# Kernel tuning notes

Measured on AMD Instinct MI355X. Metric: run time of the kernel, lower is better.

## Reference

```python
import jax, jax.numpy as jnp
import numpy as np

H = 2048          # hidden_size
NH = 16           # num attention heads
NKV = 4           # num kv heads (GQA)
HD = 128          # head_dim (= v_head_dim)
E = 16            # n_routed_experts
K = 4             # num_experts_per_tok
DFF = 1024        # moe_intermediate_size
G = 4             # n_group
TG = 2            # topk_group
THETA = 1000000.0
EPS = 1e-6
B, S = 1, 1024


def _rmsnorm(x, w):
    return x * jax.lax.rsqrt(jnp.mean(x * x, axis=-1, keepdims=True) + EPS) * w


def _rope(pos, x):
    # neox-style rotary, full head_dim. x: [B,S,h,HD], pos: [B,S]
    half = HD // 2
    inv_freq = 1.0 / (THETA ** (jnp.arange(half, dtype=jnp.float32) / half))
    ang = pos[..., None].astype(jnp.float32) * inv_freq          # [B,S,half]
    cos = jnp.cos(ang)[:, :, None, :]
    sin = jnp.sin(ang)[:, :, None, :]
    x1, x2 = x[..., :half], x[..., half:]
    return jnp.concatenate([x1 * cos - x2 * sin, x2 * cos + x1 * sin], axis=-1)


def setup_inputs() -> dict:
    key = jax.random.key(0)
    ks = jax.random.split(key, 10)
    sc = 0.02
    return {
        "hidden_states": jax.random.normal(ks[0], (B, S, H), dtype=jnp.float32),
        "positions": jnp.arange(B * S, dtype=jnp.int64 if jax.config.jax_enable_x64 else jnp.int32).reshape(B, S),
        "in_norm_w": jnp.ones((H,), jnp.float32),
        "post_norm_w": jnp.ones((H,), jnp.float32),
        "qkv_w": jax.random.normal(ks[1], (H, (NH + 2 * NKV) * HD), jnp.float32) * sc,
        "o_w": jax.random.normal(ks[2], (NH * HD, H), jnp.float32) * sc,
        "gate_w": jax.random.normal(ks[3], (E, H), jnp.float32) * sc,
        "gate_bias": jax.random.normal(ks[4], (E,), jnp.float32) * sc,
        "gate_up_w": jax.random.normal(ks[5], (E, H, 2 * DFF), jnp.float32) * sc,
        "down_w": jax.random.normal(ks[6], (E, DFF, H), jnp.float32) * sc,
    }


def reference(hidden_states, positions, in_norm_w, post_norm_w, qkv_w, o_w,
              gate_w, gate_bias, gate_up_w, down_w):
    Bq, Sq, _ = hidden_states.shape
    T = Bq * Sq

    # ---- pre-norm attention ----
    residual = hidden_states
    h = _rmsnorm(hidden_states, in_norm_w)
    qkv = h @ qkv_w                                             # [B,S,(NH+2*NKV)*HD]
    q, k, v = jnp.split(qkv, [NH * HD, (NH + NKV) * HD], axis=-1)
    q = q.reshape(Bq, Sq, NH, HD)
    k = k.reshape(Bq, Sq, NKV, HD)
    v = v.reshape(Bq, Sq, NKV, HD)
    q = _rope(positions, q)
    k = _rope(positions, k)
    rep = NH // NKV
    k = jnp.repeat(k, rep, axis=2)                              # [B,S,NH,HD]
    v = jnp.repeat(v, rep, axis=2)
    scores = jnp.einsum('bqhd,bkhd->bhqk', q, k) * (HD ** -0.5)
    causal = jnp.tril(jnp.ones((Sq, Sq), bool))
    scores = jnp.where(causal, scores, -1e30)
    attn = jax.nn.softmax(scores, axis=-1)
    o = jnp.einsum('bhqk,bkhd->bqhd', attn, v).reshape(Bq, Sq, NH * HD)
    h = residual + o @ o_w

    # ---- pre-norm MoE ----
    residual = h
    x = _rmsnorm(h, post_norm_w).reshape(T, H)

    # gate (fp32), sigmoid scores + correction bias, grouped top-k (noaux_tc)
    logits = x.astype(jnp.float32) @ gate_w.T                   # [T,E]
    sig = jax.nn.sigmoid(logits)
    sb = sig + gate_bias.astype(jnp.float32)
    grp = sb.reshape(T, G, E // G)
    group_scores = jax.lax.top_k(grp, 2)[0].sum(-1)             # [T,G]
    _, gidx = jax.lax.top_k(group_scores, TG)
    gmask = jax.nn.one_hot(gidx, G, dtype=sb.dtype).sum(1)      # [T,G]
    emask = jnp.repeat(gmask, E // G, axis=1)                   # [T,E]
    masked = jnp.where(emask > 0, sb, -jnp.inf)
    _, tidx = jax.lax.top_k(masked, K)                          # [T,K]
    w = jnp.take_along_axis(sig, tidx, axis=1)
    w = w / (w.sum(-1, keepdims=True) + 1e-20)                  # renormalize

    # experts: dense compute, sparse combine
    gu = jnp.einsum('td,edf->etf', x, gate_up_w)                # [E,T,2*DFF]
    g, u = jnp.split(gu, 2, axis=-1)
    act = jax.nn.silu(g) * u
    y = jnp.einsum('etf,efd->etd', act, down_w)                 # [E,T,H]
    cw = jnp.zeros((T, E), jnp.float32).at[jnp.arange(T)[:, None], tidx].add(w)
    moe_out = jnp.einsum('te,etd->td', cw, y.astype(jnp.float32))
    return residual + moe_out.astype(hidden_states.dtype).reshape(Bq, Sq, H)
```

## Files before the change

kernel.cpp:

```cpp
#include <hip/hip_runtime.h>
#include <hip/hip_bf16.h>
#include <math.h>

#define H_DIM   2048
#define NH      16
#define NKV     4
#define HD      128
#define NE      16
#define TOPK    4
#define DFF     1024
#define NG      4
#define SEQ     1024
#define QKV_N   3072
#define EPS_RMS 1e-6f
#define THETA   1000000.0f

typedef __attribute__((ext_vector_type(8))) short bf16x8;
typedef __attribute__((ext_vector_type(4))) short s16x4;
typedef __attribute__((ext_vector_type(4))) float f32x4;

__device__ inline unsigned short f2bf(float x) {
    unsigned u = __builtin_bit_cast(unsigned, x);
    unsigned r = (u + 0x7FFFu + ((u >> 16) & 1u)) >> 16;
    return (unsigned short)r;
}

__device__ inline unsigned pk2bf(float lo, float hi) {
    __hip_bfloat162 h = __float22bfloat162_rn(float2{lo, hi});
    unsigned r;
    __builtin_memcpy(&r, &h, 4);
    return r;
}

__global__ __launch_bounds__(256) void w2bfT(const float* __restrict__ in,
                                             unsigned short* __restrict__ out,
                                             int K, int N) {
    const float* src = in + (size_t)blockIdx.z * K * N;
    unsigned short* dst = out + (size_t)blockIdx.z * K * N;
    int n0 = blockIdx.x * 64, k0 = blockIdx.y * 64;
    __shared__ unsigned short tile[64][66];
    int tid = threadIdx.x, c = tid & 63, r4 = tid >> 6;
    #pragma unroll
    for (int rep = 0; rep < 16; rep++) {
        int r = rep * 4 + r4;
        tile[r][c] = f2bf(src[(size_t)(k0 + r) * N + n0 + c]);
    }
    __syncthreads();
    #pragma unroll
    for (int rep = 0; rep < 16; rep++) {
        int r = rep * 4 + r4;
        dst[(size_t)(n0 + r) * K + k0 + c] = tile[c][r];
    }
}

__global__ __launch_bounds__(256) void rmsnorm_dual(const float* __restrict__ in,
                                                    const float* __restrict__ w,
                                                    float* __restrict__ outf,
                                                    unsigned short* __restrict__ outb) {
    int t = blockIdx.x;
    const float* xt = in + (size_t)t * H_DIM;
    float ss = 0.f;
    for (int d = threadIdx.x * 4; d < H_DIM; d += 1024) {
        float4 v = *reinterpret_cast<const float4*>(xt + d);
        ss += v.x * v.x + v.y * v.y + v.z * v.z + v.w * v.w;
    }
    for (int off = 1; off < 64; off <<= 1) ss += __shfl_xor(ss, off);
    __shared__ float red[4];
    __shared__ float srms;
    if ((threadIdx.x & 63) == 0) red[threadIdx.x >> 6] = ss;
    __syncthreads();
    if (threadIdx.x == 0)
        srms = rsqrtf((red[0] + red[1] + red[2] + red[3]) * (1.f / H_DIM) + EPS_RMS);
    __syncthreads();
    float r = srms;
    for (int d = threadIdx.x * 4; d < H_DIM; d += 1024) {
        float4 v  = *reinterpret_cast<const float4*>(xt + d);
        float4 wv = *reinterpret_cast<const float4*>(w + d);
        float4 ov;
        ov.x = v.x * r * wv.x; ov.y = v.y * r * wv.y;
        ov.z = v.z * r * wv.z; ov.w = v.w * r * wv.w;
        if (outf) *reinterpret_cast<float4*>(outf + (size_t)t * H_DIM + d) = ov;
        if (outb) {
            s16x4 bv = (s16x4){(short)f2bf(ov.x), (short)f2bf(ov.y),
                               (short)f2bf(ov.z), (short)f2bf(ov.w)};
            *reinterpret_cast<s16x4*>(outb + (size_t)t * H_DIM + d) = bv;
        }
    }
}

__global__ __launch_bounds__(128) void gemm_qkv_rope(const unsigned short* __restrict__ A,
                                                     const unsigned short* __restrict__ Bt,
                                                     const int* __restrict__ positions,
                                                     unsigned short* __restrict__ Qb,
                                                     unsigned short* __restrict__ Kb,
                                                     unsigned short* __restrict__ Vt) {
    __shared__ unsigned short As[8][66][8];
    __shared__ unsigned short Bs[8][130][8];
    int xb = blockIdx.x;
    int row0 = blockIdx.y * 64, col0 = xb * 128;
    int t = threadIdx.x;
    int w = t >> 6, lane = t & 63, lo = lane & 15, g = lane >> 4;
    int wr = w * 32;
    f32x4 acc[2][8];
    #pragma unroll
    for (int mi = 0; mi < 2; mi++)
        #pragma unroll
        for (int ni = 0; ni < 8; ni++) acc[mi][ni] = (f32x4){0.f, 0.f, 0.f, 0.f};
    int arow8 = t >> 3, ac = t & 7;
    size_t aoff[4], boff[8];
    #pragma unroll
    for (int rep = 0; rep < 4; rep++)
        aoff[rep] = (size_t)(row0 + rep * 16 + arow8) * H_DIM + ac * 8;
    #pragma unroll
    for (int rep = 0; rep < 8; rep++)
        boff[rep] = (size_t)(col0 + rep * 16 + arow8) * H_DIM + ac * 8;
    bf16x8 aR[4], bR[8];
    #pragma unroll
    for (int rep = 0; rep < 4; rep++) aR[rep] = *(const bf16x8*)(A + aoff[rep]);
    #pragma unroll
    for (int rep = 0; rep < 8; rep++) bR[rep] = *(const bf16x8*)(Bt + boff[rep]);
    for (int k0 = 0; k0 < H_DIM; k0 += 64) {
        #pragma unroll
        for (int rep = 0; rep < 4; rep++)
            *(bf16x8*)As[ac][rep * 16 + arow8] = aR[rep];
        #pragma unroll
        for (int rep = 0; rep < 8; rep++)
            *(bf16x8*)Bs[ac][rep * 16 + arow8] = bR[rep];
        int kn = k0 + 64;
        if (kn < H_DIM) {
            #pragma unroll
            for (int rep = 0; rep < 4; rep++) aR[rep] = *(const bf16x8*)(A + aoff[rep] + kn);
            #pragma unroll
            for (int rep = 0; rep < 8; rep++) bR[rep] = *(const bf16x8*)(Bt + boff[rep] + kn);
        }
        __syncthreads();
        #pragma unroll
        for (int kh = 0; kh < 2; kh++) {
            bf16x8 af[2], bfr[8];
            #pragma unroll
            for (int mi = 0; mi < 2; mi++) af[mi] = *(const bf16x8*)As[kh * 4 + g][wr + mi * 16 + lo];
            #pragma unroll
            for (int ni = 0; ni < 8; ni++) bfr[ni] = *(const bf16x8*)Bs[kh * 4 + g][ni * 16 + lo];
            #pragma unroll
            for (int mi = 0; mi < 2; mi++)
                #pragma unroll
                for (int ni = 0; ni < 8; ni++)
                    acc[mi][ni] = __builtin_amdgcn_mfma_f32_16x16x32_bf16(af[mi], bfr[ni], acc[mi][ni], 0, 0, 0);
        }
        __syncthreads();
    }
    if (xb < NH + NKV) {
        bool isQ = (xb < NH);
        unsigned short* dst = isQ ? (Qb + (size_t)xb * SEQ * HD)
                                  : (Kb + (size_t)(xb - NH) * SEQ * HD);
        float qs = isQ ? 0.08838834764831845f : 1.0f;
        float invf[4];
        #pragma unroll
        for (int ni = 0; ni < 4; ni++)
            invf[ni] = __powf(THETA, -(float)(ni * 16 + lo) * (1.0f / 64.0f));
        #pragma unroll
        for (int mi = 0; mi < 2; mi++)
            #pragma unroll
            for (int r = 0; r < 4; r++) {
                int tok = row0 + wr + mi * 16 + g * 4 + r;
                float pos = (float)positions[tok];
                #pragma unroll
                for (int ni = 0; ni < 4; ni++) {
                    float s, c;
                    __sincosf(pos * invf[ni], &s, &c);
                    float x1 = acc[mi][ni][r], x2 = acc[mi][ni + 4][r];
                    int d = ni * 16 + lo;
                    dst[(size_t)tok * HD + d]      = f2bf((x1 * c - x2 * s) * qs);
                    dst[(size_t)tok * HD + d + 64] = f2bf((x2 * c + x1 * s) * qs);
                }
            }
    } else {
        int kvh = xb - (NH + NKV);
        #pragma unroll
        for (int mi = 0; mi < 2; mi++)
            #pragma unroll
            for (int ni = 0; ni < 8; ni++) {
                int tok0 = row0 + wr + mi * 16 + g * 4;
                int d = ni * 16 + lo;
                ushort4 v4;
                v4.x = f2bf(acc[mi][ni][0]);
                v4.y = f2bf(acc[mi][ni][1]);
                v4.z = f2bf(acc[mi][ni][2]);
                v4.w = f2bf(acc[mi][ni][3]);
                *reinterpret_cast<ushort4*>(Vt + ((size_t)kvh * HD + d) * SEQ + tok0) = v4;
            }
    }
}

__global__ __launch_bounds__(256) void gemm_bf16(const unsigned short* __restrict__ A,
                                                 const unsigned short* __restrict__ Bt,
                                                 float* __restrict__ C,
                                                 float* __restrict__ C2,
                                                 const float* __restrict__ R,
                                                 int M, int N, int K) {
    __shared__ unsigned short As[8][130][8];
    __shared__ unsigned short Bs[8][66][8];
    int row0 = blockIdx.y * 128, col0 = blockIdx.x * 64;
    int t = threadIdx.x;
    int w = t >> 6, lane = t & 63, lo = lane & 15, g = lane >> 4;
    int wr = (w >> 1) * 64, wc = (w & 1) * 32;
    f32x4 acc[4][2];
    #pragma unroll
    for (int mi = 0; mi < 4; mi++)
        #pragma unroll
        for (int ni = 0; ni < 2; ni++) acc[mi][ni] = (f32x4){0.f, 0.f, 0.f, 0.f};
    int arow8 = t >> 3, ac = t & 7;
    size_t aoff[4], boff[2];
    #pragma unroll
    for (int rep = 0; rep < 4; rep++)
        aoff[rep] = (size_t)(row0 + rep * 32 + arow8) * K + ac * 8;
    #pragma unroll
    for (int rep = 0; rep < 2; rep++)
        boff[rep] = (size_t)(col0 + rep * 32 + arow8) * K + ac * 8;
    bf16x8 aR[4], bR[2];
    #pragma unroll
    for (int rep = 0; rep < 4; rep++) aR[rep] = *(const bf16x8*)(A + aoff[rep]);
    #pragma unroll
    for (int rep = 0; rep < 2; rep++) bR[rep] = *(const bf16x8*)(Bt + boff[rep]);
    for (int k0 = 0; k0 < K; k0 += 64) {
        #pragma unroll
        for (int rep = 0; rep < 4; rep++)
            *(bf16x8*)As[ac][rep * 32 + arow8] = aR[rep];
        #pragma unroll
        for (int rep = 0; rep < 2; rep++)
            *(bf16x8*)Bs[ac][rep * 32 + arow8] = bR[rep];
        int kn = k0 + 64;
        if (kn < K) {
            #pragma unroll
            for (int rep = 0; rep < 4; rep++) aR[rep] = *(const bf16x8*)(A + aoff[rep] + kn);
            #pragma unroll
            for (int rep = 0; rep < 2; rep++) bR[rep] = *(const bf16x8*)(Bt + boff[rep] + kn);
        }
        __syncthreads();
        #pragma unroll
        for (int kh = 0; kh < 2; kh++) {
            bf16x8 af[4], bfr[2];
            #pragma unroll
            for (int mi = 0; mi < 4; mi++) af[mi] = *(const bf16x8*)As[kh * 4 + g][wr + mi * 16 + lo];
            #pragma unroll
            for (int ni = 0; ni < 2; ni++) bfr[ni] = *(const bf16x8*)Bs[kh * 4 + g][wc + ni * 16 + lo];
            #pragma unroll
            for (int mi = 0; mi < 4; mi++)
                #pragma unroll
                for (int ni = 0; ni < 2; ni++)
                    acc[mi][ni] = __builtin_amdgcn_mfma_f32_16x16x32_bf16(af[mi], bfr[ni], acc[mi][ni], 0, 0, 0);
        }
        __syncthreads();
    }
    #pragma unroll
    for (int mi = 0; mi < 4; mi++)
        #pragma unroll
        for (int ni = 0; ni < 2; ni++)
            #pragma unroll
            for (int r = 0; r < 4; r++) {
                int row = row0 + wr + mi * 16 + g * 4 + r;
                int col = col0 + wc + ni * 16 + lo;
                size_t idx = (size_t)row * N + col;
                float v = acc[mi][ni][r];
                if (R)  v += R[idx];
                C[idx] = v;
                if (C2) C2[idx] = v;
            }
}

__global__ __launch_bounds__(128) void attn_mfma(const unsigned short* __restrict__ Qb,
                                                 const unsigned short* __restrict__ Kb,
                                                 const unsigned short* __restrict__ Vt,
                                                 unsigned short* __restrict__ ob) {
    int bx = blockIdx.x;
    int h  = blockIdx.y;
    int kvh = h >> 2;
    int wid = threadIdx.x >> 6;
    int qt = wid ? (SEQ / 16 - 1 - bx) : bx;
    int q0 = qt * 16;
    int l = threadIdx.x & 63;
    int lo = l & 15, g = l >> 4;

    __shared__ alignas(16) unsigned short pbuf[2][16][40];

    bf16x8 qf[4];
    const unsigned short* qp = Qb + ((size_t)h * SEQ + q0 + lo) * HD + g * 8;
    #pragma unroll
    for (int ks = 0; ks < 4; ks++)
        qf[ks] = *(const bf16x8*)(qp + ks * 32);

    f32x4 accO[8];
    #pragma unroll
    for (int nd = 0; nd < 8; nd++) accO[nd] = (f32x4){0.f, 0.f, 0.f, 0.f};
    float mrun[4], lrun[4];
    #pragma unroll
    for (int r = 0; r < 4; r++) { mrun[r] = -INFINITY; lrun[r] = 0.f; }

    int nc = (q0 + 16 + 31) / 32;
    for (int ch = 0; ch < nc; ch++) {
        int kv0 = ch * 32;
        f32x4 accS[2];
        accS[0] = (f32x4){0.f, 0.f, 0.f, 0.f};
        accS[1] = (f32x4){0.f, 0.f, 0.f, 0.f};
        const unsigned short* kp = Kb + ((size_t)kvh * SEQ + kv0 + lo) * HD + g * 8;
        #pragma unroll
        for (int n = 0; n < 2; n++) {
            const unsigned short* kpn = kp + (size_t)n * 16 * HD;
            #pragma unroll
            for (int ks = 0; ks < 4; ks++) {
                bf16x8 kf = *(const bf16x8*)(kpn + ks * 32);
                accS[n] = __builtin_amdgcn_mfma_f32_16x16x32_bf16(qf[ks], kf, accS[n], 0, 0, 0);
            }
        }
        if (ch == nc - 1) {
            #pragma unroll
            for (int n = 0; n < 2; n++)
                #pragma unroll
                for (int r = 0; r < 4; r++) {
                    int kv = kv0 + n * 16 + lo;
                    int q  = q0 + g * 4 + r;
                    if (kv > q) accS[n][r] = -1e30f;
                }
        }
        float mt[4], fac[4];
        #pragma unroll
        for (int r = 0; r < 4; r++) {
            float m = fmaxf(accS[0][r], accS[1][r]);
            #pragma unroll
            for (int off = 1; off < 16; off <<= 1) m = fmaxf(m, __shfl_xor(m, off));
            mt[r] = fmaxf(mrun[r], m);
            fac[r] = __expf(mrun[r] - mt[r]);
        }
        float psum[4] = {0.f, 0.f, 0.f, 0.f};
        #pragma unroll
        for (int n = 0; n < 2; n++)
            #pragma unroll
            for (int r = 0; r < 4; r++) {
                float p = __expf(accS[n][r] - mt[r]);
                psum[r] += p;
                pbuf[wid][g * 4 + r][n * 16 + lo] = f2bf(p);
            }
        #pragma unroll
        for (int r = 0; r < 4; r++) {
            float s = psum[r];
            #pragma unroll
            for (int off = 1; off < 16; off <<= 1) s += __shfl_xor(s, off);
            lrun[r] = lrun[r] * fac[r] + s;
            mrun[r] = mt[r];
        }
        #pragma unroll
        for (int nd = 0; nd < 8; nd++)
            #pragma unroll
            for (int r = 0; r < 4; r++) accO[nd][r] *= fac[r];
        __builtin_amdgcn_sched_barrier(0);
        bf16x8 pf = *(const bf16x8*)(&pbuf[wid][lo][g * 8]);
        const unsigned short* vp = Vt + ((size_t)kvh * HD + lo) * SEQ + kv0 + g * 8;
        #pragma unroll
        for (int nd = 0; nd < 8; nd++) {
            bf16x8 vf = *(const bf16x8*)(vp + (size_t)nd * 16 * SEQ);
            accO[nd] = __builtin_amdgcn_mfma_f32_16x16x32_bf16(pf, vf, accO[nd], 0, 0, 0);
        }
        __builtin_amdgcn_sched_barrier(0);
    }
    float inv[4];
    #pragma unroll
    for (int r = 0; r < 4; r++) inv[r] = 1.0f / lrun[r];
    #pragma unroll
    for (int nd = 0; nd < 8; nd++)
        #pragma unroll
        for (int r = 0; r < 4; r++)
            ob[(size_t)(q0 + g * 4 + r) * H_DIM + h * HD + nd * 16 + lo] = f2bf(accO[nd][r] * inv[r]);
}

__global__ __launch_bounds__(256) void router_kernel(const float* __restrict__ x,
                                                     const float* __restrict__ gate_w,
                                                     const float* __restrict__ gate_bias,
                                                     int* __restrict__ toklist,
                                                     float* __restrict__ tokw,
                                                     int* __restrict__ cnt) {
    int t = blockIdx.x;
    const float* xt = x + (size_t)t * H_DIM;
    __shared__ float logits[NE];
    int wid = threadIdx.x >> 6, lane = threadIdx.x & 63;
    #pragma unroll
    for (int i = 0; i < 4; i++) {
        int e = wid * 4 + i;
        const float* gw = gate_w + (size_t)e * H_DIM;
        float p = 0.f;
        for (int d = lane * 4; d < H_DIM; d += 256) {
            float4 xv = *reinterpret_cast<const float4*>(xt + d);
            float4 wv = *reinterpret_cast<const float4*>(gw + d);
            p += xv.x * wv.x + xv.y * wv.y + xv.z * wv.z + xv.w * wv.w;
        }
        #pragma unroll
        for (int off = 1; off < 64; off <<= 1) p += __shfl_xor(p, off);
        if (lane == 0) logits[e] = p;
    }
    __syncthreads();
    if (threadIdx.x == 0) {
        float sig[NE], sb[NE];
        for (int e = 0; e < NE; e++) {
            sig[e] = 1.f / (1.f + expf(-logits[e]));
            sb[e] = sig[e] + gate_bias[e];
        }
        float gs[NG];
        for (int g = 0; g < NG; g++) {
            float m1 = -1e30f, m2 = -1e30f;
            for (int i = 0; i < 4; i++) {
                float v = sb[g * 4 + i];
                if (v > m1) { m2 = m1; m1 = v; } else if (v > m2) m2 = v;
            }
            gs[g] = m1 + m2;
        }
        int g1 = 0;
        for (int g = 1; g < NG; g++) if (gs[g] > gs[g1]) g1 = g;
        int g2 = -1;
        for (int g = 0; g < NG; g++) {
            if (g == g1) continue;
            if (g2 < 0 || gs[g] > gs[g2]) g2 = g;
        }
        bool allowed[NE], used[NE];
        for (int e = 0; e < NE; e++) { int g = e >> 2; allowed[e] = (g == g1 || g == g2); used[e] = false; }
        int sel[TOPK]; float wsel[TOPK]; float wsum = 0.f;
        for (int k = 0; k < TOPK; k++) {
            int best = -1; float bv = -1e30f;
            for (int e = 0; e < NE; e++) {
                if (!allowed[e] || used[e]) continue;
                if (best < 0 || sb[e] > bv) { best = e; bv = sb[e]; }
            }
            used[best] = true; sel[k] = best; wsel[k] = sig[best]; wsum += sig[best];
        }
        float invs = 1.f / (wsum + 1e-20f);
        for (int k = 0; k < TOPK; k++) {
            int e = sel[k];
            int slot = atomicAdd(&cnt[e], 1);
            toklist[e * SEQ + slot] = t;
            tokw[e * SEQ + slot] = wsel[k] * invs;
        }
    }
}

__global__ void prefix_kernel(const int* __restrict__ cnt, int* __restrict__ base) {
    if (threadIdx.x == 0) {
        int s = 0;
        for (int e = 0; e < NE; e++) { base[e] = s; s += cnt[e]; }
    }
}

__global__ __launch_bounds__(256, 2) void moe_gemm1_mfma(const unsigned short* __restrict__ xb,
                                                         const float* __restrict__ gup,
                                                         const int* __restrict__ toklist,
                                                         const int* __restrict__ cnt,
                                                         const int* __restrict__ base,
                                                         unsigned short* __restrict__ act) {
    int e = blockIdx.z;
    int ce = cnt[e];
    int t0 = blockIdx.y * 256;
    if (t0 >= ce) return;
    int f0 = blockIdx.x * 32;
    __shared__ unsigned short As[8][258][8];
    __shared__ unsigned short BsG[8][33][8];
    __shared__ unsigned short BsU[8][33][8];
    __shared__ int toks[256];
    int t = threadIdx.x;
    { int s = t0 + t; toks[t] = toklist[e * SEQ + (s < ce ? s : 0)]; }
    __syncthreads();
    int w = t >> 6, lane = t & 63, lo = lane & 15, g = lane >> 4;
    int wrb = w * 64;
    f32x4 accG[4][2], accU[4][2];
    #pragma unroll
    for (int mi = 0; mi < 4; mi++)
        #pragma unroll
        for (int ni = 0; ni < 2; ni++) {
            accG[mi][ni] = (f32x4){0.f, 0.f, 0.f, 0.f};
            accU[mi][ni] = (f32x4){0.f, 0.f, 0.f, 0.f};
        }
    int arow8 = t >> 3, ac = t & 7;
    size_t abase[8];
    #pragma unroll
    for (int rep = 0; rep < 8; rep++)
        abase[rep] = (size_t)toks[rep * 32 + arow8] * H_DIM + ac * 8;
    int half = t >> 7, tt = t & 127;
    int rp = tt >> 3, nq = tt & 7;
    int kgB = rp >> 2, wq = (rp & 3) * 2;
    unsigned short (*Bsel)[33][8] = half ? BsU : BsG;
    const float* W = gup + (size_t)e * H_DIM * (2 * DFF);
    const float* pB0 = W + (size_t)(2 * rp) * (2 * DFF) + half * DFF + f0 + nq * 4;
    bf16x8 aR[8];
    #pragma unroll
    for (int rep = 0; rep < 8; rep++) aR[rep] = *(const bf16x8*)(xb + abase[rep]);
    f32x4 bR0 = *(const f32x4*)pB0;
    f32x4 bR1 = *(const f32x4*)(pB0 + 2 * DFF);
    f32x4 bR2 = *(const f32x4*)(pB0 + (size_t)32 * 2 * DFF);
    f32x4 bR3 = *(const f32x4*)(pB0 + (size_t)33 * 2 * DFF);
    for (int k0 = 0; k0 < H_DIM; k0 += 64) {
        #pragma unroll
        for (int rep = 0; rep < 8; rep++)
            *(bf16x8*)As[ac][rep * 32 + arow8] = aR[rep];
        #pragma unroll
        for (int j = 0; j < 4; j++) {
            *(unsigned*)&Bsel[kgB][nq * 4 + j][wq]     = pk2bf(bR0[j], bR1[j]);
            *(unsigned*)&Bsel[kgB + 4][nq * 4 + j][wq] = pk2bf(bR2[j], bR3[j]);
        }
        int kn = k0 + 64;
        if (kn < H_DIM) {
            #pragma unroll
            for (int rep = 0; rep < 8; rep++)
                aR[rep] = *(const bf16x8*)(xb + abase[rep] + kn);
            const float* pB = pB0 + (size_t)kn * (2 * DFF);
            bR0 = *(const f32x4*)pB;
            bR1 = *(const f32x4*)(pB + 2 * DFF);
            bR2 = *(const f32x4*)(pB + (size_t)32 * 2 * DFF);
            bR3 = *(const f32x4*)(pB + (size_t)33 * 2 * DFF);
        }
        __syncthreads();
        #pragma unroll
        for (int kh = 0; kh < 2; kh++) {
            bf16x8 af[4], bg[2], bu[2];
            #pragma unroll
            for (int mi = 0; mi < 4; mi++) af[mi] = *(const bf16x8*)As[kh * 4 + g][wrb + mi * 16 + lo];
            #pragma unroll
            for (int ni = 0; ni < 2; ni++) {
                bg[ni] = *(const bf16x8*)BsG[kh * 4 + g][ni * 16 + lo];
                bu[ni] = *(const bf16x8*)BsU[kh * 4 + g][ni * 16 + lo];
            }
            #pragma unroll
            for (int mi = 0; mi < 4; mi++)
                #pragma unroll
                for (int ni = 0; ni < 2; ni++) {
                    accG[mi][ni] = __builtin_amdgcn_mfma_f32_16x16x32_bf16(af[mi], bg[ni], accG[mi][ni], 0, 0, 0);
                    accU[mi][ni] = __builtin_amdgcn_mfma_f32_16x16x32_bf16(af[mi], bu[ni], accU[mi][ni], 0, 0, 0);
                }
        }
        __syncthreads();
    }
    int b = base[e];
    #pragma unroll
    for (int mi = 0; mi < 4; mi++)
        #pragma unroll
        for (int ni = 0; ni < 2; ni++)
            #pragma unroll
            for (int r = 0; r < 4; r++) {
                int slot = t0 + wrb + mi * 16 + g * 4 + r;
                if (slot < ce) {
                    float gv = accG[mi][ni][r], uv = accU[mi][ni][r];
                    float a = (gv / (1.f + __expf(-gv))) * uv;
                    act[(size_t)(b + slot) * DFF + f0 + ni * 16 + lo] = f2bf(a);
                }
            }
}

__global__ __launch_bounds__(256, 4) void moe_gemm2_mfma(const unsigned short* __restrict__ act,
                                                         const float* __restrict__ down,
                                                         const int* __restrict__ toklist,
                                                         const float* __restrict__ tokw,
                                                         const int* __restrict__ cnt,
                                                         const int* __restrict__ base,
                                                         float* __restrict__ out) {
    int e = blockIdx.z;
    int ce = cnt[e];
    int t0 = blockIdx.y * 256;
    if (t0 >= ce) return;
    int c0 = blockIdx.x * 32;
    __shared__ unsigned short As[8][258][8];
    __shared__ unsigned short Bs[8][33][8];
    int t = threadIdx.x;
    int w = t >> 6, lane = t & 63, lo = lane & 15, g = lane >> 4;
    int wrb = w * 64;
    int b = base[e];
    f32x4 acc[4][2];
    #pragma unroll
    for (int mi = 0; mi < 4; mi++)
        #pragma unroll
        for (int ni = 0; ni < 2; ni++) acc[mi][ni] = (f32x4){0.f, 0.f, 0.f, 0.f};
    int arow8 = t >> 3, ac = t & 7;
    size_t abase[8];
    #pragma unroll
    for (int rep = 0; rep < 8; rep++) {
        int slot = t0 + rep * 32 + arow8;
        abase[rep] = (size_t)(b + (slot < ce ? slot : t0)) * DFF + ac * 8;
    }
    int tt = t & 127;
    int rp = tt >> 3, nq = tt & 7;
    int kgB = rp >> 2, wq = (rp & 3) * 2;
    const float* pB0 = down + (size_t)e * DFF * H_DIM + (size_t)(2 * rp) * H_DIM + c0 + nq * 4;
    bool stageB = (t < 128);
    bf16x8 aR[8];
    #pragma unroll
    for (int rep = 0; rep < 8; rep++) aR[rep] = *(const bf16x8*)(act + abase[rep]);
    f32x4 bR0 = (f32x4){0.f,0.f,0.f,0.f}, bR1 = bR0, bR2 = bR0, bR3 = bR0;
    if (stageB) {
        bR0 = *(const f32x4*)pB0;
        bR1 = *(const f32x4*)(pB0 + H_DIM);
        bR2 = *(const f32x4*)(pB0 + (size_t)32 * H_DIM);
        bR3 = *(const f32x4*)(pB0 + (size_t)33 * H_DIM);
    }
    for (int k0 = 0; k0 < DFF; k0 += 64) {
        #pragma unroll
        for (int rep = 0; rep < 8; rep++)
            *(bf16x8*)As[ac][rep * 32 + arow8] = aR[rep];
        if (stageB) {
            #pragma unroll
            for (int j = 0; j < 4; j++) {
                *(unsigned*)&Bs[kgB][nq * 4 + j][wq]     = pk2bf(bR0[j], bR1[j]);
                *(unsigned*)&Bs[kgB + 4][nq * 4 + j][wq] = pk2bf(bR2[j], bR3[j]);
            }
        }
        int kn = k0 + 64;
        if (kn < DFF) {
            #pragma unroll
            for (int rep = 0; rep < 8; rep++)
                aR[rep] = *(const bf16x8*)(act + abase[rep] + kn);
            if (stageB) {
                const float* pB = pB0 + (size_t)kn * H_DIM;
                bR0 = *(const f32x4*)pB;
                bR1 = *(const f32x4*)(pB + H_DIM);
                bR2 = *(const f32x4*)(pB + (size_t)32 * H_DIM);
                bR3 = *(const f32x4*)(pB + (size_t)33 * H_DIM);
            }
        }
        __syncthreads();
        #pragma unroll
        for (int kh = 0; kh < 2; kh++) {
            bf16x8 af[4], bfr[2];
            #pragma unroll
            for (int mi = 0; mi < 4; mi++) af[mi] = *(const bf16x8*)As[kh * 4 + g][wrb + mi * 16 + lo];
            #pragma unroll
            for (int ni = 0; ni < 2; ni++) bfr[ni] = *(const bf16x8*)Bs[kh * 4 + g][ni * 16 + lo];
            #pragma unroll
            for (int mi = 0; mi < 4; mi++)
                #pragma unroll
                for (int ni = 0; ni < 2; ni++)
                    acc[mi][ni] = __builtin_amdgcn_mfma_f32_16x16x32_bf16(af[mi], bfr[ni], acc[mi][ni], 0, 0, 0);
        }
        __syncthreads();
    }
    #pragma unroll
    for (int mi = 0; mi < 4; mi++)
        #pragma unroll
        for (int r = 0; r < 4; r++) {
            int slot = t0 + wrb + mi * 16 + g * 4 + r;
            if (slot < ce) {
                int tok = toklist[e * SEQ + slot];
                float wt = tokw[e * SEQ + slot];
                #pragma unroll
                for (int ni = 0; ni < 2; ni++)
                    atomicAdd(&out[(size_t)tok * H_DIM + c0 + ni * 16 + lo],
                              wt * acc[mi][ni][r]);
            }
        }
}

extern "C" void kernel_launch(void* const* d_in, const int* in_sizes, int n_in,
                              void* d_out, int out_size, void* d_ws, size_t ws_size,
                              hipStream_t stream) {
    const float* hidden     = (const float*)d_in[0];
    const int*   positions  = (const int*)d_in[1];
    const float* in_norm_w  = (const float*)d_in[2];
    const float* post_norm_w= (const float*)d_in[3];
    const float* qkv_w      = (const float*)d_in[4];
    const float* o_w        = (const float*)d_in[5];
    const float* gate_w     = (const float*)d_in[6];
    const float* gate_bias  = (const float*)d_in[7];
    const float* gate_up_w  = (const float*)d_in[8];
    const float* down_w     = (const float*)d_in[9];
    float* out = (float*)d_out;

    float* ws   = (float*)d_ws;
    float* h2   = ws;
    float* x    = h2  + (size_t)SEQ * H_DIM;
    float* tokw = x   + (size_t)SEQ * H_DIM;
    int* toklist = (int*)(tokw + NE * SEQ);
    int* cnt  = toklist + NE * SEQ;
    int* base = cnt + NE;
    unsigned short* hb = (unsigned short*)(base + NE);
    unsigned short* ob = hb + (size_t)SEQ * H_DIM;
    unsigned short* xbuf = ob + (size_t)SEQ * H_DIM;
    unsigned short* act = xbuf + (size_t)SEQ * H_DIM;
    unsigned short* Qb = act + (size_t)4 * SEQ * DFF;
    unsigned short* Kb = Qb + (size_t)NH * SEQ * HD;
    unsigned short* Vt = Kb + (size_t)NKV * SEQ * HD;
    unsigned short* qkvT = Vt + (size_t)NKV * HD * SEQ;
    unsigned short* oT   = qkvT + (size_t)QKV_N * H_DIM;

    w2bfT<<<dim3(QKV_N / 64, H_DIM / 64, 1), 256, 0, stream>>>(qkv_w, qkvT, H_DIM, QKV_N);
    w2bfT<<<dim3(H_DIM / 64, H_DIM / 64, 1), 256, 0, stream>>>(o_w, oT, H_DIM, H_DIM);

    rmsnorm_dual<<<SEQ, 256, 0, stream>>>(hidden, in_norm_w, nullptr, hb);
    gemm_qkv_rope<<<dim3(QKV_N / 128, SEQ / 64), 128, 0, stream>>>(hb, qkvT, positions, Qb, Kb, Vt);
    attn_mfma<<<dim3(SEQ / 32, NH), 128, 0, stream>>>(Qb, Kb, Vt, ob);
    gemm_bf16<<<dim3(H_DIM / 64, SEQ / 128), 256, 0, stream>>>(ob, oT, h2, out, hidden,
                                                               SEQ, H_DIM, H_DIM);
    rmsnorm_dual<<<SEQ, 256, 0, stream>>>(h2, post_norm_w, x, xbuf);
    (void)hipMemsetAsync(cnt, 0, NE * sizeof(int), stream);
    router_kernel<<<SEQ, 256, 0, stream>>>(x, gate_w, gate_bias, toklist, tokw, cnt);
    prefix_kernel<<<1, 64, 0, stream>>>(cnt, base);
    moe_gemm1_mfma<<<dim3(DFF / 32, SEQ / 256, NE), 256, 0, stream>>>(xbuf, gate_up_w, toklist, cnt, base, act);
    moe_gemm2_mfma<<<dim3(H_DIM / 32, SEQ / 256, NE), 256, 0, stream>>>(act, down_w, toklist, tokw, cnt, base, out);
}
```

Before: 401.8 us.

## Split attention KV chunks across two waves per query tile and merge via LDS

Doubles the attention block to 256 threads so each query tile's KV chunks are divided between two waves. Each wave keeps its own online-softmax state. The second wave writes its partial output, max and sum into shared memory, and the first wave merges them with rescaling before writing bf16 output. This shortens the serial KV loop per wave and raises the number of waves available to hide latency. In exchange it adds LDS traffic, a block-wide barrier, and more shared memory per block.

Result: faster. 382.5 us, median of 3 (-4.8%).

```diff
diff --git a/kernel.cpp b/kernel.cpp
--- a/kernel.cpp
+++ b/kernel.cpp
@@ -268,20 +268,24 @@
             }
 }
 
-__global__ __launch_bounds__(128) void attn_mfma(const unsigned short* __restrict__ Qb,
+__global__ __launch_bounds__(256) void attn_mfma(const unsigned short* __restrict__ Qb,
                                                  const unsigned short* __restrict__ Kb,
                                                  const unsigned short* __restrict__ Vt,
                                                  unsigned short* __restrict__ ob) {
     int bx = blockIdx.x;
     int h  = blockIdx.y;
     int kvh = h >> 2;
-    int wid = threadIdx.x >> 6;
-    int qt = wid ? (SEQ / 16 - 1 - bx) : bx;
+    int tid = threadIdx.x;
+    int wid = tid >> 6;
+    int qsel = wid >> 1, khalf = wid & 1;
+    int qt = qsel ? (SEQ / 16 - 1 - bx) : bx;
     int q0 = qt * 16;
-    int l = threadIdx.x & 63;
+    int l = tid & 63;
     int lo = l & 15, g = l >> 4;
 
-    __shared__ alignas(16) unsigned short pbuf[2][16][40];
+    __shared__ alignas(16) unsigned short pbuf[4][16][40];
+    __shared__ float obuf[2][16][128];
+    __shared__ float mbuf[2][16], lbuf[2][16];
 
     bf16x8 qf[4];
     const unsigned short* qp = Qb + ((size_t)h * SEQ + q0 + lo) * HD + g * 8;
@@ -297,7 +301,10 @@
     for (int r = 0; r < 4; r++) { mrun[r] = -INFINITY; lrun[r] = 0.f; }
 
     int nc = (q0 + 16 + 31) / 32;
-    for (int ch = 0; ch < nc; ch++) {
+    int ncH = (nc + 1) >> 1;
+    int cbeg = khalf ? ncH : 0;
+    int cend = khalf ? nc : ncH;
+    for (int ch = cbeg; ch < cend; ch++) {
         int kv0 = ch * 32;
         f32x4 accS[2];
         accS[0] = (f32x4){0.f, 0.f, 0.f, 0.f};
@@ -362,14 +369,36 @@
         }
         __builtin_amdgcn_sched_barrier(0);
     }
-    float inv[4];
-    #pragma unroll
-    for (int r = 0; r < 4; r++) inv[r] = 1.0f / lrun[r];
-    #pragma unroll
-    for (int nd = 0; nd < 8; nd++)
-        #pragma unroll
-        for (int r = 0; r < 4; r++)
-            ob[(size_t)(q0 + g * 4 + r) * H_DIM + h * HD + nd * 16 + lo] = f2bf(accO[nd][r] * inv[r]);
+    if (khalf) {
+        #pragma unroll
+        for (int r = 0; r < 4; r++) {
+            if (lo == 0) {
+                mbuf[qsel][g * 4 + r] = mrun[r];
+                lbuf[qsel][g * 4 + r] = lrun[r];
+            }
+            #pragma unroll
+            for (int nd = 0; nd < 8; nd++)
+                obuf[qsel][g * 4 + r][nd * 16 + lo] = accO[nd][r];
+        }
+    }
+    __syncthreads();
+    if (!khalf) {
+        #pragma unroll
+        for (int r = 0; r < 4; r++) {
+            int row = g * 4 + r;
+            float m1 = mbuf[qsel][row], l1 = lbuf[qsel][row];
+            float m0 = mrun[r], l0 = lrun[r];
+            float m = fmaxf(m0, m1);
+            float f0 = (l0 > 0.f) ? __expf(m0 - m) : 0.f;
+            float f1 = (l1 > 0.f) ? __expf(m1 - m) : 0.f;
+            float linv = 1.f / (l0 * f0 + l1 * f1);
+            #pragma unroll
+            for (int nd = 0; nd < 8; nd++) {
+                float v = (accO[nd][r] * f0 + obuf[qsel][row][nd * 16 + lo] * f1) * linv;
+                ob[(size_t)(q0 + row) * H_DIM + h * HD + nd * 16 + lo] = f2bf(v);
+            }
+        }
+    }
 }
 
 __global__ __launch_bounds__(256) void router_kernel(const float* __restrict__ x,
@@ -688,7 +717,7 @@
 
     rmsnorm_dual<<<SEQ, 256, 0, stream>>>(hidden, in_norm_w, nullptr, hb);
     gemm_qkv_rope<<<dim3(QKV_N / 128, SEQ / 64), 128, 0, stream>>>(hb, qkvT, positions, Qb, Kb, Vt);
-    attn_mfma<<<dim3(SEQ / 32, NH), 128, 0, stream>>>(Qb, Kb, Vt, ob);
+    attn_mfma<<<dim3(SEQ / 32, NH), 256, 0, stream>>>(Qb, Kb, Vt, ob);
     gemm_bf16<<<dim3(H_DIM / 64, SEQ / 128), 256, 0, stream>>>(ob, oT, h2, out, hidden,
                                                                SEQ, H_DIM, H_DIM);
     rmsnorm_dual<<<SEQ, 256, 0, stream>>>(h2, post_norm_w, x, xbuf);
```
